# Kernel optimization log

Measured on AMD Instinct MI355X. Metric: run time of the kernel, lower is better.

Reference implementation:

```python
import jax, jax.numpy as jnp
import numpy as np

N_BINS = 18
TEMP = 0.01  # n_phases > 1e7 so effective_temperature = 0.01 (same as init default)
EPS = 1e-10  # fp16=False
PI = np.pi


def setup_inputs() -> dict:
    key = jax.random.key(0)
    k1, k2 = jax.random.split(key)
    B, C, P, A, S, T = 4, 8, 20, 30, 4, 2048
    phase = jax.random.uniform(k1, (B, C, P, S, T), jnp.float32, -PI, PI)
    amplitude = jax.random.uniform(k2, (B, C, A, S, T), jnp.float32, 0.0, 1.0)
    return {"phase": phase, "amplitude": amplitude}


def reference(phase, amplitude):
    # phase:     (B, C, Fp, S, T)
    # amplitude: (B, C, Fa, S, T)
    edges = jnp.linspace(-PI, PI, N_BINS + 1).astype(phase.dtype)
    centers = (edges[1:] + edges[:-1]) * 0.5  # (N,)

    # Soft phase binning: circular distance to each bin center, softmax over bins.
    diff = phase[..., None] - centers  # (B, C, Fp, S, T, N)
    diff = jnp.fmod(diff + PI, 2.0 * PI) - PI  # torch.fmod = truncated mod = jnp.fmod
    weights = jax.nn.softmax(-jnp.abs(diff) / TEMP, axis=-1)  # (B, C, Fp, S, T, N)

    # Amplitude-weighted histogram: contract over time.
    # dist: (B, C, Fp, Fa, S, N)
    dist = jnp.einsum('bcpstn,bcast->bcpasn', weights, amplitude)

    # Normalize to a distribution over bins, clamp, Shannon entropy.
    p = dist / (dist.sum(axis=-1, keepdims=True) + EPS)
    p = jnp.maximum(p, EPS)
    neg_entropy = (p * jnp.log(p)).sum(axis=-1)  # (B, C, Fp, Fa, S)

    mi = 1.0 + neg_entropy / jnp.log(jnp.asarray(N_BINS, dtype=p.dtype))
    # -> (B, C, S, Fp, Fa) to match torch output layout
    return jnp.transpose(mi, (0, 1, 4, 2, 3))
```

## Files before the change

### kernel.cpp

```cpp
#include <hip/hip_runtime.h>
#include <math.h>
#include <stdint.h>

#define BB 4
#define CC 8
#define PP 20
#define AA 30
#define SS 4
#define TT 2048
#define NB 18

#define TC 128
#define NCH (TT / TC)
#define PG 2
#define NPG (PP / PG)
#define WSTR 132
#define WROWS 19
#define NTH 256

#define BAR() do { asm volatile("s_waitcnt lgkmcnt(0)" ::: "memory"); \
                   __builtin_amdgcn_s_barrier(); } while (0)

typedef _Float16 half4_t __attribute__((ext_vector_type(4)));
typedef _Float16 half8_t __attribute__((ext_vector_type(8)));
typedef float f32x16 __attribute__((ext_vector_type(16)));

__device__ __forceinline__ void weight_top2(float x, int& n0, int& n1,
                                            float& w0, float& w1)
{
    const float PI_F  = 3.14159265358979323846f;
    const float INV_H = 2.8647913f;
    float u = (x + PI_F) * INV_H;
    n0 = (int)floorf(u);
    n0 = n0 < 0 ? 0 : (n0 > NB - 1 ? NB - 1 : n0);
    float f  = u - (float)n0 - 0.5f;
    float af = fabsf(f);
    n1 = n0 + (f >= 0.0f ? 1 : -1);
    float e;
    if (n1 < 0) {
        e = 0.0f; n1 = NB;
    } else {
        if (n1 == NB) n1 = 0;
        e = __expf(fmaf(af, 69.81317008f, -34.90658504f));
    }
    w0 = __builtin_amdgcn_rcpf(1.0f + e);
    w1 = 1.0f - w0;
}

__global__ __launch_bounds__(NTH, 5)
void mi_fused_kernel(const float* __restrict__ phase,
                     const float* __restrict__ amp,
                     float* __restrict__ out)
{
    __shared__ __align__(16) _Float16 lds[2 * WROWS * WSTR + 2 * AA * WSTR];
    _Float16* const Wl0 = lds;
    _Float16* const Wl1 = lds + WROWS * WSTR;
    _Float16* const amp0 = lds + 2 * WROWS * WSTR;

    const int tid = threadIdx.x;
    const int bid = blockIdx.x;
    const int x   = bid & 7;
    const int kk  = bid >> 3;
    const int pg  = kk % NPG;
    const int g   = x + 8 * (kk / NPG);
    const int s   = g & (SS - 1);
    const int bc  = g >> 2;

    const int kh   = tid >> 6;
    const int lane = tid & 63;
    const int mrow = lane & 31;
    const int mlh  = lane >> 5;
    const int arow = mrow < WROWS ? mrow : (WROWS - 1);
    const int brow = mrow < AA    ? mrow : (AA - 1);
    const int col  = kh * 32 + mrow;
    _Float16* const ptile = mlh ? Wl1 : Wl0;

    const float* am  = amp + (size_t)bc * (AA * SS * TT) + (size_t)s * TT;
    const float* phl = phase + ((size_t)(bc * PP + pg * PG + mlh) * SS + s) * TT + col;

    for (int i = tid; i < 627; i += NTH)
        ((uint4*)lds)[i] = make_uint4(0u, 0u, 0u, 0u);
    #pragma unroll
    for (int j = 0; j < 4; ++j) {
        int q = tid + j * NTH;
        int a = q >> 5, tq = q & 31;
        if (a < AA) {
            const float4 v = *(const float4*)&am[(size_t)a * (SS * TT) + tq * 4];
            half4_t h = { (_Float16)v.x, (_Float16)v.y, (_Float16)v.z, (_Float16)v.w };
            *(half4_t*)&amp0[a * WSTR + tq * 4] = h;
        }
    }
    float phv = phl[0];
    BAR();

    f32x16 acc0 = {}, acc1 = {};
    int pn0 = 0, pn1 = 0;

    for (int c = 0; c < NCH; ++c) {
        const int cb = c & 1, tb = cb ^ 1;
        const _Float16* aB = amp0 + cb * (AA * WSTR);
        _Float16* aW = amp0 + tb * (AA * WSTR);

        float nphv = 0.0f;
        float4 stg[4];
        if (c + 1 < NCH) {
            nphv = phl[(c + 1) * TC];
            #pragma unroll
            for (int j = 0; j < 4; ++j) {
                int q = tid + j * NTH;
                int a = q >> 5, tq = q & 31;
                int ac = a < AA ? a : (AA - 1);
                stg[j] = *(const float4*)&am[(size_t)ac * (SS * TT) + (c + 1) * TC + tq * 4];
            }
        }

        if (c > 0) {
            ptile[pn0 * WSTR + col] = (_Float16)0.0f;
            ptile[pn1 * WSTR + col] = (_Float16)0.0f;
        }
        {
            int n0, n1; float w0, w1;
            weight_top2(phv, n0, n1, w0, w1);
            ptile[n0 * WSTR + col] = (_Float16)w0;
            ptile[n1 * WSTR + col] = (_Float16)w1;
            pn0 = n0; pn1 = n1;
        }

        __builtin_amdgcn_s_setprio(1);
        #pragma unroll
        for (int ks = 0; ks < 2; ++ks) {
            int t0 = kh * 32 + ks * 16 + mlh * 8;
            const _Float16* Bb  = aB  + brow * WSTR + t0;
            const _Float16* A0b = Wl0 + arow * WSTR + t0;
            const _Float16* A1b = Wl1 + arow * WSTR + t0;
            half4_t b0 = *(const half4_t*)Bb;
            half4_t b1 = *(const half4_t*)(Bb + 4);
            half4_t p0a = *(const half4_t*)A0b;
            half4_t p0b = *(const half4_t*)(A0b + 4);
            half4_t p1a = *(const half4_t*)A1b;
            half4_t p1b = *(const half4_t*)(A1b + 4);
            half8_t bv  = __builtin_shufflevector(b0, b1, 0, 1, 2, 3, 4, 5, 6, 7);
            half8_t a0v = __builtin_shufflevector(p0a, p0b, 0, 1, 2, 3, 4, 5, 6, 7);
            half8_t a1v = __builtin_shufflevector(p1a, p1b, 0, 1, 2, 3, 4, 5, 6, 7);
            acc0 = __builtin_amdgcn_mfma_f32_32x32x16_f16(a0v, bv, acc0, 0, 0, 0);
            acc1 = __builtin_amdgcn_mfma_f32_32x32x16_f16(a1v, bv, acc1, 0, 0, 0);
        }
        __builtin_amdgcn_s_setprio(0);

        if (c + 1 < NCH) {
            #pragma unroll
            for (int j = 0; j < 4; ++j) {
                int q = tid + j * NTH;
                int a = q >> 5, tq = q & 31;
                if (a < AA) {
                    half4_t h = { (_Float16)stg[j].x, (_Float16)stg[j].y,
                                  (_Float16)stg[j].z, (_Float16)stg[j].w };
                    *(half4_t*)&aW[a * WSTR + tq * 4] = h;
                }
            }
        }
        phv = nphv;
        BAR();
    }

    float* const df = (float*)lds;
    #pragma unroll
    for (int r = 0; r < 16; ++r) {
        int row = (r & 3) + 8 * (r >> 2) + 4 * mlh;
        if (row < NB) {
            df[(kh * 2 + 0) * 576 + row * 32 + mrow] = acc0[r];
            df[(kh * 2 + 1) * 576 + row * 32 + mrow] = acc1[r];
        }
    }
    BAR();

    if (kh < PG && lane < AA) {
        float v[NB], tot = 0.0f;
        #pragma unroll
        for (int n = 0; n < NB; ++n) {
            v[n] = df[(0 * 2 + kh) * 576 + n * 32 + lane]
                 + df[(1 * 2 + kh) * 576 + n * 32 + lane]
                 + df[(2 * 2 + kh) * 576 + n * 32 + lane]
                 + df[(3 * 2 + kh) * 576 + n * 32 + lane];
            tot += v[n];
        }
        float inv = 1.0f / (tot + 1e-10f);
        float ne = 0.0f;
        #pragma unroll
        for (int n = 0; n < NB; ++n) {
            float pv = fmaxf(v[n] * inv, 1e-10f);
            ne += pv * logf(pv);
        }
        out[((size_t)(bc * SS + s) * PP + pg * PG + kh) * AA + lane] =
            1.0f + ne * 0.345975362f;
    }
}

extern "C" void kernel_launch(void* const* d_in, const int* in_sizes, int n_in,
                              void* d_out, int out_size, void* d_ws, size_t ws_size,
                              hipStream_t stream)
{
    const float* phase = (const float*)d_in[0];
    const float* amp   = (const float*)d_in[1];
    float* out = (float*)d_out;
    hipLaunchKernelGGL(mi_fused_kernel, dim3(BB * CC * SS * NPG), dim3(NTH),
                       0, stream, phase, amp, out);
}
```

Before: 28.21 us.

## Load amplitude straight into MFMA registers and drop per-chunk LDS barriers

Each lane now reads its own amplitude values from global memory, converts them to half and feeds them directly as the B operand of the MFMA. This replaces the double-buffered LDS staging of amplitude. Because each wave only reads and writes its own columns of the weight tile, the block-wide barrier in every chunk is removed, as is the bulk zero-init, now a per-lane clear of the lane's own column. The cost is that the global loads are issued at the top of each iteration with no software prefetch, so their latency may be exposed. A separate LDS array is also added for the final reduction.

```diff
diff --git a/kernel.cpp b/kernel.cpp
--- a/kernel.cpp
+++ b/kernel.cpp
@@ -52,10 +52,8 @@
                      const float* __restrict__ amp,
                      float* __restrict__ out)
 {
-    __shared__ __align__(16) _Float16 lds[2 * WROWS * WSTR + 2 * AA * WSTR];
-    _Float16* const Wl0 = lds;
-    _Float16* const Wl1 = lds + WROWS * WSTR;
-    _Float16* const amp0 = lds + 2 * WROWS * WSTR;
+    __shared__ __align__(16) _Float16 Wl[PG][WROWS * WSTR];
+    __shared__ __align__(16) float    df[8 * 576];
 
     const int tid = threadIdx.x;
     const int bid = blockIdx.x;
@@ -73,46 +71,28 @@
     const int arow = mrow < WROWS ? mrow : (WROWS - 1);
     const int brow = mrow < AA    ? mrow : (AA - 1);
     const int col  = kh * 32 + mrow;
-    _Float16* const ptile = mlh ? Wl1 : Wl0;
+    _Float16* const ptile = &Wl[mlh][0];
 
-    const float* am  = amp + (size_t)bc * (AA * SS * TT) + (size_t)s * TT;
+    const float* bp  = amp + (size_t)bc * (AA * SS * TT) + (size_t)s * TT
+                           + (size_t)brow * (SS * TT) + kh * 32 + mlh * 8;
     const float* phl = phase + ((size_t)(bc * PP + pg * PG + mlh) * SS + s) * TT + col;
 
-    for (int i = tid; i < 627; i += NTH)
-        ((uint4*)lds)[i] = make_uint4(0u, 0u, 0u, 0u);
     #pragma unroll
-    for (int j = 0; j < 4; ++j) {
-        int q = tid + j * NTH;
-        int a = q >> 5, tq = q & 31;
-        if (a < AA) {
-            const float4 v = *(const float4*)&am[(size_t)a * (SS * TT) + tq * 4];
-            half4_t h = { (_Float16)v.x, (_Float16)v.y, (_Float16)v.z, (_Float16)v.w };
-            *(half4_t*)&amp0[a * WSTR + tq * 4] = h;
-        }
-    }
+    for (int r = 0; r < WROWS; ++r)
+        ptile[r * WSTR + col] = (_Float16)0.0f;
     float phv = phl[0];
-    BAR();
 
     f32x16 acc0 = {}, acc1 = {};
     int pn0 = 0, pn1 = 0;
 
+    #pragma unroll 1
     for (int c = 0; c < NCH; ++c) {
-        const int cb = c & 1, tb = cb ^ 1;
-        const _Float16* aB = amp0 + cb * (AA * WSTR);
-        _Float16* aW = amp0 + tb * (AA * WSTR);
-
-        float nphv = 0.0f;
-        float4 stg[4];
-        if (c + 1 < NCH) {
-            nphv = phl[(c + 1) * TC];
-            #pragma unroll
-            for (int j = 0; j < 4; ++j) {
-                int q = tid + j * NTH;
-                int a = q >> 5, tq = q & 31;
-                int ac = a < AA ? a : (AA - 1);
-                stg[j] = *(const float4*)&am[(size_t)ac * (SS * TT) + (c + 1) * TC + tq * 4];
-            }
-        }
+        const float* bpc = bp + c * TC;
+        float4 f00 = *(const float4*)(bpc);
+        float4 f01 = *(const float4*)(bpc + 4);
+        float4 f10 = *(const float4*)(bpc + 16);
+        float4 f11 = *(const float4*)(bpc + 20);
+        float nphv = (c + 1 < NCH) ? phl[(c + 1) * TC] : 0.0f;
 
         if (c > 0) {
             ptile[pn0 * WSTR + col] = (_Float16)0.0f;
@@ -126,44 +106,31 @@
             pn0 = n0; pn1 = n1;
         }
 
+        half8_t bv0 = { (_Float16)f00.x, (_Float16)f00.y, (_Float16)f00.z, (_Float16)f00.w,
+                        (_Float16)f01.x, (_Float16)f01.y, (_Float16)f01.z, (_Float16)f01.w };
+        half8_t bv1 = { (_Float16)f10.x, (_Float16)f10.y, (_Float16)f10.z, (_Float16)f10.w,
+                        (_Float16)f11.x, (_Float16)f11.y, (_Float16)f11.z, (_Float16)f11.w };
+
         __builtin_amdgcn_s_setprio(1);
         #pragma unroll
         for (int ks = 0; ks < 2; ++ks) {
             int t0 = kh * 32 + ks * 16 + mlh * 8;
-            const _Float16* Bb  = aB  + brow * WSTR + t0;
-            const _Float16* A0b = Wl0 + arow * WSTR + t0;
-            const _Float16* A1b = Wl1 + arow * WSTR + t0;
-            half4_t b0 = *(const half4_t*)Bb;
-            half4_t b1 = *(const half4_t*)(Bb + 4);
+            const _Float16* A0b = &Wl[0][arow * WSTR + t0];
+            const _Float16* A1b = &Wl[1][arow * WSTR + t0];
             half4_t p0a = *(const half4_t*)A0b;
             half4_t p0b = *(const half4_t*)(A0b + 4);
             half4_t p1a = *(const half4_t*)A1b;
             half4_t p1b = *(const half4_t*)(A1b + 4);
-            half8_t bv  = __builtin_shufflevector(b0, b1, 0, 1, 2, 3, 4, 5, 6, 7);
             half8_t a0v = __builtin_shufflevector(p0a, p0b, 0, 1, 2, 3, 4, 5, 6, 7);
             half8_t a1v = __builtin_shufflevector(p1a, p1b, 0, 1, 2, 3, 4, 5, 6, 7);
+            half8_t bv  = ks ? bv1 : bv0;
             acc0 = __builtin_amdgcn_mfma_f32_32x32x16_f16(a0v, bv, acc0, 0, 0, 0);
             acc1 = __builtin_amdgcn_mfma_f32_32x32x16_f16(a1v, bv, acc1, 0, 0, 0);
         }
         __builtin_amdgcn_s_setprio(0);
-
-        if (c + 1 < NCH) {
-            #pragma unroll
-            for (int j = 0; j < 4; ++j) {
-                int q = tid + j * NTH;
-                int a = q >> 5, tq = q & 31;
-                if (a < AA) {
-                    half4_t h = { (_Float16)stg[j].x, (_Float16)stg[j].y,
-                                  (_Float16)stg[j].z, (_Float16)stg[j].w };
-                    *(half4_t*)&aW[a * WSTR + tq * 4] = h;
-                }
-            }
-        }
         phv = nphv;
-        BAR();
     }
 
-    float* const df = (float*)lds;
     #pragma unroll
     for (int r = 0; r < 16; ++r) {
         int row = (r & 3) + 8 * (r >> 2) + 4 * mlh;
```

Result: slower. 42.04 us (+49.0%).
